# Kernel tuning notes

Measured on AMD Instinct MI355X. Metric: run time of the kernel, lower is better.

The kernel has to match this reference:

```python
import jax, jax.numpy as jnp
import numpy as np
import math

B, TT, TS, C, H, L = 8, 256, 512, 512, 8, 10
HD = C // H
TOPK_FRAME = 64
# layer schedule mirrors MultimodalTransformer.forward tower order:
# 4 stimulus cross-attn (kv=frames, topk), 2 causal self-attn, 2 history cross-attn, 2 causal self-attn
# kv_source: 0=frames, 1=self, 2=id_prev
SCHED = [(0, False, TOPK_FRAME)] * 4 + [(1, True, None)] * 2 + [(2, False, None)] * 2 + [(1, True, None)] * 2


def setup_inputs() -> dict:
    key = jax.random.key(0)
    ks = jax.random.split(key, 4)
    kws = jax.random.split(ks[3], 6)
    w = lambda k, s: jax.random.normal(k, s, jnp.float32) * 0.02
    return {
        "id_x": jax.random.normal(ks[0], (B, TT, C), jnp.float32),
        "id_prev": jax.random.normal(ks[1], (B, TT, C), jnp.float32),
        "frames": jax.random.normal(ks[2], (B, TS, C), jnp.float32),
        "Wq": w(kws[0], (L, C, C)), "bq": jnp.zeros((L, C), jnp.float32),
        "Wk": w(kws[1], (L, C, C)), "bk": jnp.zeros((L, C), jnp.float32),
        "Wv": w(kws[2], (L, C, C)), "bv": jnp.zeros((L, C), jnp.float32),
        "Wo": w(kws[3], (L, C, C)), "bo": jnp.zeros((L, C), jnp.float32),
        "W1": w(kws[4], (L, C, 4 * C)), "b1": jnp.zeros((L, 4 * C), jnp.float32),
        "W2": w(kws[5], (L, 4 * C, C)), "b2": jnp.zeros((L, C), jnp.float32),
        "ln1_g": jnp.ones((L, C), jnp.float32), "ln1_b": jnp.zeros((L, C), jnp.float32),
        "ln2_g": jnp.ones((L, C), jnp.float32), "ln2_b": jnp.zeros((L, C), jnp.float32),
        "lnf_g": jnp.ones((L, C), jnp.float32), "lnf_b": jnp.zeros((L, C), jnp.float32),
    }


def _ln(x, g, b):
    mu = x.mean(-1, keepdims=True)
    var = ((x - mu) ** 2).mean(-1, keepdims=True)
    return (x - mu) * jax.lax.rsqrt(var + 1e-5) * g + b


def _block(x, kv, causal, topk, p):
    # Block.forward: x = x + attn(ln1(x), kv, kv, mask); x = x + mlp(ln2(x)); return ln_f(x)
    Wq, bq, Wk, bk, Wv, bv, Wo, bo, W1, b1, W2, b2, l1g, l1b, l2g, l2b, lfg, lfb = p
    Bx, Tt, Cx = x.shape
    Ts = kv.shape[1]
    h = _ln(x, l1g, l1b)
    q = (h @ Wq + bq).reshape(Bx, Tt, H, HD).transpose(0, 2, 1, 3)   # [B,H,Tt,HD]
    k = (kv @ Wk + bk).reshape(Bx, Ts, H, HD).transpose(0, 2, 1, 3)  # [B,H,Ts,HD]
    v = (kv @ Wv + bv).reshape(Bx, Ts, H, HD).transpose(0, 2, 1, 3)
    att = jnp.einsum('bhqd,bhkd->bhqk', q, k) * (1.0 / math.sqrt(HD))
    if causal:
        m = jnp.tril(jnp.ones((Tt, Ts), dtype=bool))
        att = jnp.where(m, att, -jnp.inf)
    if topk is not None and topk < Ts:
        top = jax.lax.top_k(att, topk)[0]           # [B,H,Tt,topk]
        att = jnp.where(att < top[..., -1:], -jnp.inf, att)
    w_att = jax.nn.softmax(att, axis=-1)
    y = jnp.einsum('bhqk,bhkd->bhqd', w_att, v).transpose(0, 2, 1, 3).reshape(Bx, Tt, Cx)
    x = x + y @ Wo + bo
    h2 = _ln(x, l2g, l2b)
    x = x + jax.nn.gelu(h2 @ W1 + b1, approximate=False) @ W2 + b2
    return _ln(x, lfg, lfb)


def _forward(id_x, id_prev, frames, Wq, bq, Wk, bk, Wv, bv, Wo, bo, W1, b1, W2, b2,
             ln1_g, ln1_b, ln2_g, ln2_b, lnf_g, lnf_b):
    x = id_x
    for i, (src, causal, topk) in enumerate(SCHED):
        kv = (frames, x, id_prev)[src]
        p = (Wq[i], bq[i], Wk[i], bk[i], Wv[i], bv[i], Wo[i], bo[i],
             W1[i], b1[i], W2[i], b2[i],
             ln1_g[i], ln1_b[i], ln2_g[i], ln2_b[i], lnf_g[i], lnf_b[i])
        x = _block(x, kv, causal, topk, p)
    return x


def reference(id_x, id_prev, frames, Wq, bq, Wk, bk, Wv, bv, Wo, bo, W1, b1, W2, b2,
              ln1_g, ln1_b, ln2_g, ln2_b, lnf_g, lnf_b):
    return _forward(id_x, id_prev, frames, Wq, bq, Wk, bk, Wv, bv, Wo, bo, W1, b1, W2, b2,
                    ln1_g, ln1_b, ln2_g, ln2_b, lnf_g, lnf_b)
```

## Files before the change

kernel.cpp:

```cpp
#include <hip/hip_runtime.h>
#include <math.h>

#define CC 512
#define NH 8
#define HD 64
#define TT 256

typedef __attribute__((ext_vector_type(8))) short short8v;
typedef __attribute__((ext_vector_type(4))) float f32x4;

__device__ inline unsigned short bfc(float f) {
  unsigned u = __float_as_uint(f);
  return (unsigned short)((u + 0x7fffu + ((u >> 16) & 1u)) >> 16);
}
__device__ inline float b2f(unsigned short s) {
  return __uint_as_float((unsigned)s << 16);
}
__device__ inline void gld16(const void* g, void* l) {
  __builtin_amdgcn_global_load_lds(
      (const __attribute__((address_space(1))) unsigned int*)g,
      (__attribute__((address_space(3))) unsigned int*)l, 16, 0, 0);
}

__global__ __launch_bounds__(256) void prep_k(const float* __restrict__ id_x,
    const float* __restrict__ frames, const float* __restrict__ id_prev,
    float* __restrict__ x, unsigned short* __restrict__ fb,
    unsigned short* __restrict__ pb) {
  int i = blockIdx.x * 256 + threadIdx.x;
  if (i < 262144) {
    ((float4*)x)[i] = ((const float4*)id_x)[i];
  } else if (i < 786432) {
    int j = i - 262144;
    float4 f = ((const float4*)frames)[j];
    ushort4 o; o.x = bfc(f.x); o.y = bfc(f.y); o.z = bfc(f.z); o.w = bfc(f.w);
    ((ushort4*)fb)[j] = o;
  } else {
    int j = i - 786432;
    float4 f = ((const float4*)id_prev)[j];
    ushort4 o; o.x = bfc(f.x); o.y = bfc(f.y); o.z = bfc(f.z); o.w = bfc(f.w);
    ((ushort4*)pb)[j] = o;
  }
}

__global__ __launch_bounds__(256) void ln_bf(const float* __restrict__ in,
    unsigned short* __restrict__ out, const float* __restrict__ g, const float* __restrict__ b) {
  int row = (blockIdx.x << 2) + (threadIdx.x >> 6), lane = threadIdx.x & 63;
  const float* r = in + (size_t)row * CC;
  float4 v0 = *(const float4*)(r + (lane << 2));
  float4 v1 = *(const float4*)(r + 256 + (lane << 2));
  float s = v0.x + v0.y + v0.z + v0.w + v1.x + v1.y + v1.z + v1.w;
  #pragma unroll
  for (int o = 32; o; o >>= 1) s += __shfl_xor(s, o);
  float mu = s * (1.0f / CC);
  float d0x = v0.x - mu, d0y = v0.y - mu, d0z = v0.z - mu, d0w = v0.w - mu;
  float d1x = v1.x - mu, d1y = v1.y - mu, d1z = v1.z - mu, d1w = v1.w - mu;
  float sq = d0x*d0x + d0y*d0y + d0z*d0z + d0w*d0w + d1x*d1x + d1y*d1y + d1z*d1z + d1w*d1w;
  #pragma unroll
  for (int o = 32; o; o >>= 1) sq += __shfl_xor(sq, o);
  float inv = rsqrtf(sq * (1.0f / CC) + 1e-5f);
  float4 g0 = *(const float4*)(g + (lane << 2)), g1 = *(const float4*)(g + 256 + (lane << 2));
  float4 b0 = *(const float4*)(b + (lane << 2)), b1 = *(const float4*)(b + 256 + (lane << 2));
  ushort4 o0, o1;
  o0.x = bfc(d0x*inv*g0.x + b0.x); o0.y = bfc(d0y*inv*g0.y + b0.y);
  o0.z = bfc(d0z*inv*g0.z + b0.z); o0.w = bfc(d0w*inv*g0.w + b0.w);
  o1.x = bfc(d1x*inv*g1.x + b1.x); o1.y = bfc(d1y*inv*g1.y + b1.y);
  o1.z = bfc(d1z*inv*g1.z + b1.z); o1.w = bfc(d1w*inv*g1.w + b1.w);
  *(ushort4*)(out + (size_t)row * CC + (lane << 2)) = o0;
  *(ushort4*)(out + (size_t)row * CC + 256 + (lane << 2)) = o1;
}

__global__ __launch_bounds__(256) void ln_final(const float* __restrict__ in,
    float* __restrict__ out, const float* __restrict__ g, const float* __restrict__ b) {
  int row = (blockIdx.x << 2) + (threadIdx.x >> 6), lane = threadIdx.x & 63;
  const float* r = in + (size_t)row * CC;
  float4 v0 = *(const float4*)(r + (lane << 2));
  float4 v1 = *(const float4*)(r + 256 + (lane << 2));
  float s = v0.x + v0.y + v0.z + v0.w + v1.x + v1.y + v1.z + v1.w;
  #pragma unroll
  for (int o = 32; o; o >>= 1) s += __shfl_xor(s, o);
  float mu = s * (1.0f / CC);
  float d0x = v0.x - mu, d0y = v0.y - mu, d0z = v0.z - mu, d0w = v0.w - mu;
  float d1x = v1.x - mu, d1y = v1.y - mu, d1z = v1.z - mu, d1w = v1.w - mu;
  float sq = d0x*d0x + d0y*d0y + d0z*d0z + d0w*d0w + d1x*d1x + d1y*d1y + d1z*d1z + d1w*d1w;
  #pragma unroll
  for (int o = 32; o; o >>= 1) sq += __shfl_xor(sq, o);
  float inv = rsqrtf(sq * (1.0f / CC) + 1e-5f);
  float4 g0 = *(const float4*)(g + (lane << 2)), g1 = *(const float4*)(g + 256 + (lane << 2));
  float4 b0 = *(const float4*)(b + (lane << 2)), b1 = *(const float4*)(b + 256 + (lane << 2));
  float4 o0, o1;
  o0.x = d0x*inv*g0.x + b0.x; o0.y = d0y*inv*g0.y + b0.y;
  o0.z = d0z*inv*g0.z + b0.z; o0.w = d0w*inv*g0.w + b0.w;
  o1.x = d1x*inv*g1.x + b1.x; o1.y = d1y*inv*g1.y + b1.y;
  o1.z = d1z*inv*g1.z + b1.z; o1.w = d1w*inv*g1.w + b1.w;
  *(float4*)(out + (size_t)row * CC + (lane << 2)) = o0;
  *(float4*)(out + (size_t)row * CC + 256 + (lane << 2)) = o1;
}

__global__ __launch_bounds__(256) void ln_chain(const float* __restrict__ in,
    float* __restrict__ xout, unsigned short* __restrict__ xb,
    const float* __restrict__ gf, const float* __restrict__ bf,
    const float* __restrict__ g1, const float* __restrict__ b1,
    unsigned short* __restrict__ hout) {
  int row = (blockIdx.x << 2) + (threadIdx.x >> 6), lane = threadIdx.x & 63;
  const float* r = in + (size_t)row * CC;
  float4 v0 = *(const float4*)(r + (lane << 2));
  float4 v1 = *(const float4*)(r + 256 + (lane << 2));
  float s = v0.x + v0.y + v0.z + v0.w + v1.x + v1.y + v1.z + v1.w;
  #pragma unroll
  for (int o = 32; o; o >>= 1) s += __shfl_xor(s, o);
  float mu = s * (1.0f / CC);
  float d0x = v0.x - mu, d0y = v0.y - mu, d0z = v0.z - mu, d0w = v0.w - mu;
  float d1x = v1.x - mu, d1y = v1.y - mu, d1z = v1.z - mu, d1w = v1.w - mu;
  float sq = d0x*d0x + d0y*d0y + d0z*d0z + d0w*d0w + d1x*d1x + d1y*d1y + d1z*d1z + d1w*d1w;
  #pragma unroll
  for (int o = 32; o; o >>= 1) sq += __shfl_xor(sq, o);
  float inv = rsqrtf(sq * (1.0f / CC) + 1e-5f);
  float4 g0 = *(const float4*)(gf + (lane << 2)), g1v = *(const float4*)(gf + 256 + (lane << 2));
  float4 b0 = *(const float4*)(bf + (lane << 2)), b1v = *(const float4*)(bf + 256 + (lane << 2));
  float4 x0, x1;
  x0.x = d0x*inv*g0.x + b0.x; x0.y = d0y*inv*g0.y + b0.y;
  x0.z = d0z*inv*g0.z + b0.z; x0.w = d0w*inv*g0.w + b0.w;
  x1.x = d1x*inv*g1v.x + b1v.x; x1.y = d1y*inv*g1v.y + b1v.y;
  x1.z = d1z*inv*g1v.z + b1v.z; x1.w = d1w*inv*g1v.w + b1v.w;
  *(float4*)(xout + (size_t)row * CC + (lane << 2)) = x0;
  *(float4*)(xout + (size_t)row * CC + 256 + (lane << 2)) = x1;
  ushort4 xb0, xb1;
  xb0.x = bfc(x0.x); xb0.y = bfc(x0.y); xb0.z = bfc(x0.z); xb0.w = bfc(x0.w);
  xb1.x = bfc(x1.x); xb1.y = bfc(x1.y); xb1.z = bfc(x1.z); xb1.w = bfc(x1.w);
  *(ushort4*)(xb + (size_t)row * CC + (lane << 2)) = xb0;
  *(ushort4*)(xb + (size_t)row * CC + 256 + (lane << 2)) = xb1;
  float s2 = x0.x + x0.y + x0.z + x0.w + x1.x + x1.y + x1.z + x1.w;
  #pragma unroll
  for (int o = 32; o; o >>= 1) s2 += __shfl_xor(s2, o);
  float mu2 = s2 * (1.0f / CC);
  float e0x = x0.x - mu2, e0y = x0.y - mu2, e0z = x0.z - mu2, e0w = x0.w - mu2;
  float e1x = x1.x - mu2, e1y = x1.y - mu2, e1z = x1.z - mu2, e1w = x1.w - mu2;
  float sq2 = e0x*e0x + e0y*e0y + e0z*e0z + e0w*e0w + e1x*e1x + e1y*e1y + e1z*e1z + e1w*e1w;
  #pragma unroll
  for (int o = 32; o; o >>= 1) sq2 += __shfl_xor(sq2, o);
  float inv2 = rsqrtf(sq2 * (1.0f / CC) + 1e-5f);
  float4 h0 = *(const float4*)(g1 + (lane << 2)), h1 = *(const float4*)(g1 + 256 + (lane << 2));
  float4 c0 = *(const float4*)(b1 + (lane << 2)), c1 = *(const float4*)(b1 + 256 + (lane << 2));
  ushort4 ho0, ho1;
  ho0.x = bfc(e0x*inv2*h0.x + c0.x); ho0.y = bfc(e0y*inv2*h0.y + c0.y);
  ho0.z = bfc(e0z*inv2*h0.z + c0.z); ho0.w = bfc(e0w*inv2*h0.w + c0.w);
  ho1.x = bfc(e1x*inv2*h1.x + c1.x); ho1.y = bfc(e1y*inv2*h1.y + c1.y);
  ho1.z = bfc(e1z*inv2*h1.z + c1.z); ho1.w = bfc(e1w*inv2*h1.w + c1.w);
  *(ushort4*)(hout + (size_t)row * CC + (lane << 2)) = ho0;
  *(ushort4*)(hout + (size_t)row * CC + 256 + (lane << 2)) = ho1;
}

__global__ __launch_bounds__(256) void transpose_w(
    const float* __restrict__ Wq, const float* __restrict__ Wk,
    const float* __restrict__ Wv, const float* __restrict__ Wo,
    const float* __restrict__ W1, const float* __restrict__ W2,
    int layer_base, unsigned short* __restrict__ wT) {
  int lz = blockIdx.x / 3072;
  int layer = layer_base + lz;
  int bid = blockIdx.x - lz * 3072;
  unsigned short* wTl = wT + (size_t)lz * 3145728;
  const float* src; unsigned short* dst; int R, Cn, tile, lg;
  if (bid < 1024) {
    int seg = bid >> 8; tile = bid & 255; R = 512; Cn = 512; lg = 4;
    const float* s4[4] = {Wq, Wk, Wv, Wo};
    src = s4[seg] + (size_t)layer * 262144;
    dst = wTl + (size_t)seg * 262144;
  } else if (bid < 2048) {
    tile = bid - 1024; R = 512; Cn = 2048; lg = 6;
    src = W1 + (size_t)layer * 1048576; dst = wTl + 1048576;
  } else {
    tile = bid - 2048; R = 2048; Cn = 512; lg = 4;
    src = W2 + (size_t)layer * 1048576; dst = wTl + 2097152;
  }
  int trb = tile >> lg, tcb = tile & ((1 << lg) - 1);
  __shared__ float tl[32][33];
  int t = threadIdx.x;
  int r = t >> 3, c4 = (t & 7) << 2;
  const float* sp = src + (size_t)(trb * 32 + r) * Cn + tcb * 32 + c4;
  float4 fv = *(const float4*)sp;
  tl[r][c4] = fv.x; tl[r][c4 + 1] = fv.y; tl[r][c4 + 2] = fv.z; tl[r][c4 + 3] = fv.w;
  __syncthreads();
  unsigned short* dp = dst + (size_t)(tcb * 32 + r) * R + trb * 32 + c4;
  ushort4 ov;
  ov.x = bfc(tl[c4][r]); ov.y = bfc(tl[c4 + 1][r]);
  ov.z = bfc(tl[c4 + 2][r]); ov.w = bfc(tl[c4 + 3][r]);
  *(ushort4*)dp = ov;
}

template<int BM, int GELU, int RES, int OUTBF, int BIAS2, int QSC>
__global__ __launch_bounds__(256) void gemm_bf(
    const unsigned short* __restrict__ A, const unsigned short* __restrict__ WT,
    const float* __restrict__ bias, const float* __restrict__ bias2,
    void* __restrict__ outp, const float* __restrict__ res, int M, int N, int K) {
  __shared__ __align__(16) unsigned short As[2][BM * 64];
  __shared__ __align__(16) unsigned short Bs[2][64 * 64];
  const int tid = threadIdx.x, lane = tid & 63, wid = tid >> 6;
  const int bm = blockIdx.y * BM, bn = blockIdx.x << 6;
  const int wm = (wid >> 1) * (BM / 2), wn = (wid & 1) << 5;
  constexpr int MF = BM / 32;
  f32x4 acc[MF][2] = {};
  const int fr = lane & 15, fq = lane >> 4;
  const int srow_a = tid >> 3, sgc = tid & 7;

  auto stage = [&](int buf, int k0) {
    #pragma unroll
    for (int i = 0; i < BM / 32; i++) {
      int row = srow_a + (i << 5);
      int gcs = sgc ^ (row & 7);
      gld16(A + (size_t)(bm + row) * K + k0 + (gcs << 3),
            (char*)As[buf] + (i << 12) + (wid << 10));
    }
    #pragma unroll
    for (int i = 0; i < 2; i++) {
      int row = srow_a + (i << 5);
      int gcs = sgc ^ (row & 7);
      gld16(WT + (size_t)(bn + row) * K + k0 + (gcs << 3),
            (char*)Bs[buf] + (i << 12) + (wid << 10));
    }
  };

  stage(0, 0);
  __syncthreads();
  int cur = 0;
  for (int k0 = 0; k0 < K; k0 += 64) {
    if (k0 + 64 < K) stage(cur ^ 1, k0 + 64);
    short8v af[MF][2], bf2[2][2];
    #pragma unroll
    for (int mf = 0; mf < MF; mf++)
      #pragma unroll
      for (int ks = 0; ks < 2; ks++) {
        int r = wm + mf * 16 + fr;
        int c = (ks << 2) + fq;
        af[mf][ks] = *(const short8v*)((const char*)As[cur] + ((((r << 7) + (c << 4))) ^ ((r & 7) << 4)));
      }
    #pragma unroll
    for (int nf = 0; nf < 2; nf++)
      #pragma unroll
      for (int ks = 0; ks < 2; ks++) {
        int r = wn + nf * 16 + fr;
        int c = (ks << 2) + fq;
        bf2[nf][ks] = *(const short8v*)((const char*)Bs[cur] + ((((r << 7) + (c << 4))) ^ ((r & 7) << 4)));
      }
    #pragma unroll
    for (int mf = 0; mf < MF; mf++)
      #pragma unroll
      for (int nf = 0; nf < 2; nf++) {
        acc[mf][nf] = __builtin_amdgcn_mfma_f32_16x16x32_bf16(af[mf][0], bf2[nf][0], acc[mf][nf], 0, 0, 0);
        acc[mf][nf] = __builtin_amdgcn_mfma_f32_16x16x32_bf16(af[mf][1], bf2[nf][1], acc[mf][nf], 0, 0, 0);
      }
    __syncthreads();
    cur ^= 1;
  }
  #pragma unroll
  for (int mf = 0; mf < MF; mf++)
    #pragma unroll
    for (int nf = 0; nf < 2; nf++) {
      int col = bn + wn + nf * 16 + fr;
      float bia = (BIAS2 && col >= 512) ? bias2[col - 512] : bias[col];
      #pragma unroll
      for (int rr = 0; rr < 4; rr++) {
        int row = bm + wm + mf * 16 + fq * 4 + rr;
        float vv = acc[mf][nf][rr] + bia;
        if (GELU) vv = 0.5f * vv * (1.0f + erff(vv * 0.70710678118654752f));
        if (RES)  vv += res[(size_t)row * N + col];
        if (QSC)  vv *= 0.125f;
        if (OUTBF) ((unsigned short*)outp)[(size_t)row * N + col] = bfc(vv);
        else       ((float*)outp)[(size_t)row * N + col] = vv;
      }
    }
}

__global__ __launch_bounds__(256) void gemm_qkv(
    const unsigned short* __restrict__ hb, const unsigned short* __restrict__ wqT,
    const float* __restrict__ bq,
    const unsigned short* __restrict__ kvA, const unsigned short* __restrict__ wkvT,
    const float* __restrict__ bk, const float* __restrict__ bv,
    unsigned short* __restrict__ qout, unsigned short* __restrict__ kvout) {
  const int tid = threadIdx.x, lane = tid & 63, wid = tid >> 6;
  int bid = blockIdx.x;
  const unsigned short *A, *WT;
  const float *bias, *bias2;
  unsigned short* outp;
  int bm, bn, N;
  bool isq = bid < 256;
  if (isq) {
    A = hb; WT = wqT; bias = bq; bias2 = bq; outp = qout; N = 512;
    bm = (bid >> 3) << 6; bn = (bid & 7) << 6;
  } else {
    int t = bid - 256;
    A = kvA; WT = wkvT; bias = bk; bias2 = bv; outp = kvout; N = 1024;
    bm = (t >> 4) << 6; bn = (t & 15) << 6;
  }
  __shared__ __align__(16) unsigned short As[2][64 * 64];
  __shared__ __align__(16) unsigned short Bs[2][64 * 64];
  const int wm = (wid >> 1) << 5, wn = (wid & 1) << 5;
  f32x4 acc[2][2] = {};
  const int fr = lane & 15, fq = lane >> 4;
  const int srow_a = tid >> 3, sgc = tid & 7;
  auto stage = [&](int buf, int k0) {
    #pragma unroll
    for (int i = 0; i < 2; i++) {
      int row = srow_a + (i << 5);
      int gcs = sgc ^ (row & 7);
      gld16(A + (size_t)(bm + row) * 512 + k0 + (gcs << 3),
            (char*)As[buf] + (i << 12) + (wid << 10));
      gld16(WT + (size_t)(bn + row) * 512 + k0 + (gcs << 3),
            (char*)Bs[buf] + (i << 12) + (wid << 10));
    }
  };
  stage(0, 0);
  __syncthreads();
  int cur = 0;
  for (int k0 = 0; k0 < 512; k0 += 64) {
    if (k0 + 64 < 512) stage(cur ^ 1, k0 + 64);
    short8v af[2][2], bf2[2][2];
    #pragma unroll
    for (int mf = 0; mf < 2; mf++)
      #pragma unroll
      for (int ks = 0; ks < 2; ks++) {
        int r = wm + mf * 16 + fr;
        int c = (ks << 2) + fq;
        af[mf][ks] = *(const short8v*)((const char*)As[cur] + ((((r << 7) + (c << 4))) ^ ((r & 7) << 4)));
        int r2 = wn + mf * 16 + fr;
        bf2[mf][ks] = *(const short8v*)((const char*)Bs[cur] + ((((r2 << 7) + (c << 4))) ^ ((r2 & 7) << 4)));
      }
    #pragma unroll
    for (int mf = 0; mf < 2; mf++)
      #pragma unroll
      for (int nf = 0; nf < 2; nf++) {
        acc[mf][nf] = __builtin_amdgcn_mfma_f32_16x16x32_bf16(af[mf][0], bf2[nf][0], acc[mf][nf], 0, 0, 0);
        acc[mf][nf] = __builtin_amdgcn_mfma_f32_16x16x32_bf16(af[mf][1], bf2[nf][1], acc[mf][nf], 0, 0, 0);
      }
    __syncthreads();
    cur ^= 1;
  }
  #pragma unroll
  for (int mf = 0; mf < 2; mf++)
    #pragma unroll
    for (int nf = 0; nf < 2; nf++) {
      int col = bn + wn + nf * 16 + fr;
      float bia = (col >= 512) ? bias2[col - 512] : bias[col];
      #pragma unroll
      for (int rr = 0; rr < 4; rr++) {
        int row = bm + wm + mf * 16 + fq * 4 + rr;
        float vv = acc[mf][nf][rr] + bia;
        if (isq) vv *= 0.125f;
        outp[(size_t)row * N + col] = bfc(vv);
      }
    }
}

template<int CAUSAL, int TOPK, int TSK>
__global__ __launch_bounds__(512, 4) void attn_m(
    const unsigned short* __restrict__ qb, const unsigned short* __restrict__ kv,
    unsigned short* __restrict__ yb) {
  constexpr int NT = TSK / 64;
  constexpr int NKC = TSK / 128;
  constexpr int SST = TSK + 8;
  constexpr int SBYTES = 8 * SST * 4;
  __shared__ __align__(16) char sm[SBYTES + 32768 + 2048];
  float* S = (float*)sm;
  char* KsB = sm + SBYTES;
  char* Qs  = sm + SBYTES + 32768;
  float* swt = (float*)KsB;
  unsigned short* kidx = (unsigned short*)(KsB + 4096);
  int tid = threadIdx.x, lane = tid & 63, wid = tid >> 6;
  int bid = blockIdx.x;
  int swz = ((bid & 7) << 8) | (bid >> 3);
  int b = swz >> 8, h = (swz >> 5) & 7, q0 = (swz & 31) << 3;
  if (tid < 64) {
    int row = tid >> 3, sp = tid & 7;
    gld16(qb + (size_t)((b << 8) + q0 + row) * CC + (h << 6) + ((sp ^ (row & 7)) << 3),
          Qs);
  } else if (tid < 128) {
    short8v z = {0, 0, 0, 0, 0, 0, 0, 0};
    *(short8v*)(Qs + (tid << 4)) = z;
  }
  const unsigned short* kgb = kv + (size_t)b * TSK * 1024 + (h << 6);
  int nte = NKC;
  if (CAUSAL) { int ub = (q0 + 8 + 127) >> 7; nte = ub < NKC ? ub : NKC; }
  auto stageK = [&](int buf, int t) {
    #pragma unroll
    for (int j = 0; j < 2; j++) {
      int s = (wid << 7) + (j << 6) + lane;
      int row = s >> 3, sp = s & 7;
      gld16(kgb + (size_t)((t << 7) + row) * 1024 + ((sp ^ (row & 7)) << 3),
            KsB + (buf << 14) + (wid << 11) + (j << 10));
    }
  };
  stageK(0, 0);
  __syncthreads();
  short8v aF[2];
  {
    int r = lane & 15, kq2 = lane >> 4;
    #pragma unroll
    for (int kc2 = 0; kc2 < 2; kc2++)
      aF[kc2] = *(const short8v*)(Qs +
                 (((r << 7) + (kc2 << 6) + (kq2 << 4)) ^ ((r & 7) << 4)));
  }
  int cur = 0;
  for (int t = 0; t < nte; t++) {
    if (t + 1 < nte) stageK(cur ^ 1, t + 1);
    int kq2 = lane >> 4;
    f32x4 acc = {};
    int key16 = (wid << 4) + (lane & 15);
    #pragma unroll
    for (int kc2 = 0; kc2 < 2; kc2++) {
      short8v bF = *(const short8v*)(KsB + (cur << 14) +
                    (((key16 << 7) + (kc2 << 6) + (kq2 << 4)) ^ ((key16 & 7) << 4)));
      acc = __builtin_amdgcn_mfma_f32_16x16x32_bf16(aF[kc2], bF, acc, 0, 0, 0);
    }
    if (kq2 < 2) {
      int col = (t << 7) + key16;
      #pragma unroll
      for (int r = 0; r < 4; r++)
        S[(kq2 * 4 + r) * SST + col] = acc[r];
    }
    __syncthreads();
    cur ^= 1;
  }
  int row = wid;
  int qi = q0 + row;
  int jmax = CAUSAL ? (qi + 1) : TSK;
  const unsigned short* vgb = kv + (size_t)b * TSK * 1024 + 512 + (h << 6) + lane;
  float sc[NT];
  float lmax = -3.0e38f;
  #pragma unroll
  for (int tt = 0; tt < NT; tt++) {
    int key = lane + (tt << 6);
    float v = (!CAUSAL || key < jmax) ? S[row * SST + key] : -3.0e38f;
    sc[tt] = v;
    lmax = fmaxf(lmax, v);
  }
  float mx = lmax;
  #pragma unroll
  for (int o = 32; o; o >>= 1) mx = fmaxf(mx, __shfl_xor(mx, o));
  float oacc = 0.f;
  if (TOPK) {
    unsigned key[NT];
    #pragma unroll
    for (int tt = 0; tt < NT; tt++) {
      unsigned u = __float_as_uint(sc[tt]);
      key[tt] = (u & 0x80000000u) ? ~u : (u | 0x80000000u);
    }
    unsigned prefix = 0u;
    for (int bit = 31; bit >= 0; bit--) {
      unsigned cand = prefix | (1u << bit);
      int cnt = 0;
      #pragma unroll
      for (int tt = 0; tt < NT; tt++)
        cnt += __popcll(__ballot(key[tt] >= cand));
      if (cnt >= 64) {
        prefix = cand;
        if (cnt == 64) break;
      }
    }
    float wvv[NT];
    float psum = 0.f;
    int basec = 0;
    #pragma unroll
    for (int tt = 0; tt < NT; tt++) {
      bool keep = key[tt] >= prefix;
      float wv = keep ? exp2f((sc[tt] - mx) * 1.4426950408889634f) : 0.f;
      wvv[tt] = wv;
      psum += wv;
      unsigned long long mask = __ballot(keep);
      if (keep) {
        int pos = basec + (int)__popcll(mask & ((1ull << lane) - 1ull));
        if (pos < 128) {
          kidx[(row << 7) + pos] = (unsigned short)(lane + (tt << 6));
          swt[(row << 7) + pos] = wv;
        }
      }
      basec += (int)__popcll(mask);
    }
    #pragma unroll
    for (int o = 32; o; o >>= 1) psum += __shfl_xor(psum, o);
    float inv = 1.0f / psum;
    int nk = basec;
    if (nk <= 128) {
      float a0 = 0.f, a1 = 0.f, a2 = 0.f, a3 = 0.f;
      int i = 0;
      for (; i + 3 < nk; i += 4) {
        a0 += swt[(row << 7) + i]     * b2f(vgb[(size_t)kidx[(row << 7) + i] * 1024]);
        a1 += swt[(row << 7) + i + 1] * b2f(vgb[(size_t)kidx[(row << 7) + i + 1] * 1024]);
        a2 += swt[(row << 7) + i + 2] * b2f(vgb[(size_t)kidx[(row << 7) + i + 2] * 1024]);
        a3 += swt[(row << 7) + i + 3] * b2f(vgb[(size_t)kidx[(row << 7) + i + 3] * 1024]);
      }
      for (; i < nk; i++) a0 += swt[(row << 7) + i] * b2f(vgb[(size_t)kidx[(row << 7) + i] * 1024]);
      oacc = (a0 + a1 + a2 + a3) * inv;
    } else {
      #pragma unroll
      for (int tt = 0; tt < NT; tt++)
        S[row * SST + lane + (tt << 6)] = wvv[tt];
      float a0 = 0.f, a1 = 0.f;
      for (int j = 0; j + 1 < TSK; j += 2) {
        a0 += S[row * SST + j]     * b2f(vgb[(size_t)j * 1024]);
        a1 += S[row * SST + j + 1] * b2f(vgb[(size_t)(j + 1) * 1024]);
      }
      oacc = (a0 + a1) * inv;
    }
  } else {
    float psum = 0.f;
    #pragma unroll
    for (int tt = 0; tt < NT; tt++) {
      int keyj = lane + (tt << 6);
      float wv = (keyj < jmax) ? exp2f((sc[tt] - mx) * 1.4426950408889634f) : 0.f;
      S[row * SST + keyj] = wv;
      psum += wv;
    }
    #pragma unroll
    for (int o = 32; o; o >>= 1) psum += __shfl_xor(psum, o);
    float inv = 1.0f / psum;
    float a0 = 0.f, a1 = 0.f, a2 = 0.f, a3 = 0.f;
    int j = 0;
    for (; j + 3 < jmax; j += 4) {
      a0 += S[row * SST + j]     * b2f(vgb[(size_t)j * 1024]);
      a1 += S[row * SST + j + 1] * b2f(vgb[(size_t)(j + 1) * 1024]);
      a2 += S[row * SST + j + 2] * b2f(vgb[(size_t)(j + 2) * 1024]);
      a3 += S[row * SST + j + 3] * b2f(vgb[(size_t)(j + 3) * 1024]);
    }
    for (; j < jmax; j++) a0 += S[row * SST + j] * b2f(vgb[(size_t)j * 1024]);
    oacc = (a0 + a1 + a2 + a3) * inv;
  }
  yb[(size_t)((b << 8) + qi) * CC + (h << 6) + lane] = bfc(oacc);
}

extern "C" void kernel_launch(void* const* d_in, const int* in_sizes, int n_in,
                              void* d_out, int out_size, void* d_ws, size_t ws_size,
                              hipStream_t stream) {
  const float* id_x    = (const float*)d_in[0];
  const float* id_prev = (const float*)d_in[1];
  const float* frames  = (const float*)d_in[2];
  const float* Wq = (const float*)d_in[3];  const float* bq = (const float*)d_in[4];
  const float* Wk = (const float*)d_in[5];  const float* bk = (const float*)d_in[6];
  const float* Wv = (const float*)d_in[7];  const float* bv = (const float*)d_in[8];
  const float* Wo = (const float*)d_in[9];  const float* bo = (const float*)d_in[10];
  const float* W1 = (const float*)d_in[11]; const float* b1 = (const float*)d_in[12];
  const float* W2 = (const float*)d_in[13]; const float* b2 = (const float*)d_in[14];
  const float* l1g = (const float*)d_in[15]; const float* l1b = (const float*)d_in[16];
  const float* l2g = (const float*)d_in[17]; const float* l2b = (const float*)d_in[18];
  const float* lfg = (const float*)d_in[19]; const float* lfb = (const float*)d_in[20];

  float* x = (float*)d_out;
  char* W  = (char*)d_ws;
  unsigned short* qbuf = (unsigned short*)W;
  unsigned short* kvb  = (unsigned short*)(W + ((size_t)4  << 20));
  unsigned short* m1b  = (unsigned short*)(W + ((size_t)4  << 20));
  unsigned short* hb   = (unsigned short*)(W + ((size_t)12 << 20));
  unsigned short* ybf  = (unsigned short*)(W + ((size_t)14 << 20));
  unsigned short* xb   = (unsigned short*)(W + ((size_t)16 << 20));
  unsigned short* fb   = (unsigned short*)(W + ((size_t)18 << 20));
  unsigned short* pb   = (unsigned short*)(W + ((size_t)22 << 20));
  unsigned short* wT   = (unsigned short*)(W + ((size_t)24 << 20));

  const bool allw = ws_size >= (((size_t)24 << 20) + (size_t)10 * 3145728 * 2);

  prep_k<<<4096, 256, 0, stream>>>(id_x, frames, id_prev, x, fb, pb);
  if (allw)
    transpose_w<<<30720, 256, 0, stream>>>(Wq, Wk, Wv, Wo, W1, W2, 0, wT);

  static const int ssrc[10] = {0, 0, 0, 0, 1, 1, 2, 2, 1, 1};

  for (int i = 0; i < 10; i++) {
    if (!allw)
      transpose_w<<<3072, 256, 0, stream>>>(Wq, Wk, Wv, Wo, W1, W2, i, wT);
    unsigned short* wTl = wT + (allw ? (size_t)i * 3145728 : 0);
    unsigned short* wqT = wTl;
    unsigned short* wkvT = wTl + 262144;
    unsigned short* woT = wTl + 786432;
    unsigned short* w1T = wTl + 1048576;
    unsigned short* w2T = wTl + 2097152;

    if (i == 0)
      ln_bf<<<512, 256, 0, stream>>>(x, hb, l1g, l1b);

    const unsigned short* kvsrc; int Mkv;
    if (ssrc[i] == 0)      { kvsrc = fb; Mkv = 4096; }
    else if (ssrc[i] == 1) { kvsrc = xb; Mkv = 2048; }
    else                   { kvsrc = pb; Mkv = 2048; }
    gemm_qkv<<<256 + (Mkv / 64) * 16, 256, 0, stream>>>(
        hb, wqT, bq + i * 512, kvsrc, wkvT, bk + i * 512, bv + i * 512, qbuf, kvb);

    if (ssrc[i] == 0)      attn_m<0, 1, 512><<<2048, 512, 0, stream>>>(qbuf, kvb, ybf);
    else if (ssrc[i] == 1) attn_m<1, 0, 256><<<2048, 512, 0, stream>>>(qbuf, kvb, ybf);
    else                   attn_m<0, 0, 256><<<2048, 512, 0, stream>>>(qbuf, kvb, ybf);

    gemm_bf<32, 0, 1, 0, 0, 0><<<dim3(8, 64), 256, 0, stream>>>(ybf, woT, bo + i * 512, nullptr, x, x, 2048, 512, 512);
    ln_bf<<<512, 256, 0, stream>>>(x, hb, l2g + i * 512, l2b + i * 512);
    gemm_bf<128, 1, 0, 1, 0, 0><<<dim3(32, 16), 256, 0, stream>>>(hb, w1T, b1 + i * 2048, nullptr, m1b, nullptr, 2048, 2048, 512);
    gemm_bf<32, 0, 1, 0, 0, 0><<<dim3(8, 64), 256, 0, stream>>>(m1b, w2T, b2 + i * 512, nullptr, x, x, 2048, 512, 2048);

    if (i < 9)
      ln_chain<<<512, 256, 0, stream>>>(x, x, xb, lfg + i * 512, lfb + i * 512,
                                        l1g + (i + 1) * 512, l1b + (i + 1) * 512, hb);
    else
      ln_final<<<512, 256, 0, stream>>>(x, x, lfg + i * 512, lfb + i * 512);
  }
}
```

Baseline: 1.016 ms.

## Fuse LayerNorm into the prologue of the Q projection and MLP-up GEMMs

Removes the standalone ln_bf launches and the second LayerNorm from ln_chain. The Q-projection GEMM and a new gemm_ln kernel for the MLP-up projection now compute per-row mean and variance from the fp32 residual and normalize A tiles in registers before writing bf16 into LDS. This saves launches and the round trip through the bf16 hb buffer. In exchange, every N-tile block recomputes row statistics and reads fp32 A instead of bf16 A. The MLP-up GEMM also moves from 128-row to 64-row tiles, and variance is now computed in one pass as E[x^2]-mu^2.

```diff
diff --git a/kernel.cpp b/kernel.cpp
--- a/kernel.cpp
+++ b/kernel.cpp
@@ -40,33 +40,6 @@
     ushort4 o; o.x = bfc(f.x); o.y = bfc(f.y); o.z = bfc(f.z); o.w = bfc(f.w);
     ((ushort4*)pb)[j] = o;
   }
-}
-
-__global__ __launch_bounds__(256) void ln_bf(const float* __restrict__ in,
-    unsigned short* __restrict__ out, const float* __restrict__ g, const float* __restrict__ b) {
-  int row = (blockIdx.x << 2) + (threadIdx.x >> 6), lane = threadIdx.x & 63;
-  const float* r = in + (size_t)row * CC;
-  float4 v0 = *(const float4*)(r + (lane << 2));
-  float4 v1 = *(const float4*)(r + 256 + (lane << 2));
-  float s = v0.x + v0.y + v0.z + v0.w + v1.x + v1.y + v1.z + v1.w;
-  #pragma unroll
-  for (int o = 32; o; o >>= 1) s += __shfl_xor(s, o);
-  float mu = s * (1.0f / CC);
-  float d0x = v0.x - mu, d0y = v0.y - mu, d0z = v0.z - mu, d0w = v0.w - mu;
-  float d1x = v1.x - mu, d1y = v1.y - mu, d1z = v1.z - mu, d1w = v1.w - mu;
-  float sq = d0x*d0x + d0y*d0y + d0z*d0z + d0w*d0w + d1x*d1x + d1y*d1y + d1z*d1z + d1w*d1w;
-  #pragma unroll
-  for (int o = 32; o; o >>= 1) sq += __shfl_xor(sq, o);
-  float inv = rsqrtf(sq * (1.0f / CC) + 1e-5f);
-  float4 g0 = *(const float4*)(g + (lane << 2)), g1 = *(const float4*)(g + 256 + (lane << 2));
-  float4 b0 = *(const float4*)(b + (lane << 2)), b1 = *(const float4*)(b + 256 + (lane << 2));
-  ushort4 o0, o1;
-  o0.x = bfc(d0x*inv*g0.x + b0.x); o0.y = bfc(d0y*inv*g0.y + b0.y);
-  o0.z = bfc(d0z*inv*g0.z + b0.z); o0.w = bfc(d0w*inv*g0.w + b0.w);
-  o1.x = bfc(d1x*inv*g1.x + b1.x); o1.y = bfc(d1y*inv*g1.y + b1.y);
-  o1.z = bfc(d1z*inv*g1.z + b1.z); o1.w = bfc(d1w*inv*g1.w + b1.w);
-  *(ushort4*)(out + (size_t)row * CC + (lane << 2)) = o0;
-  *(ushort4*)(out + (size_t)row * CC + 256 + (lane << 2)) = o1;
 }
 
 __global__ __launch_bounds__(256) void ln_final(const float* __restrict__ in,
@@ -98,9 +71,7 @@
 
 __global__ __launch_bounds__(256) void ln_chain(const float* __restrict__ in,
     float* __restrict__ xout, unsigned short* __restrict__ xb,
-    const float* __restrict__ gf, const float* __restrict__ bf,
-    const float* __restrict__ g1, const float* __restrict__ b1,
-    unsigned short* __restrict__ hout) {
+    const float* __restrict__ gf, const float* __restrict__ bf) {
   int row = (blockIdx.x << 2) + (threadIdx.x >> 6), lane = threadIdx.x & 63;
   const float* r = in + (size_t)row * CC;
   float4 v0 = *(const float4*)(r + (lane << 2));
@@ -129,25 +100,6 @@
   xb1.x = bfc(x1.x); xb1.y = bfc(x1.y); xb1.z = bfc(x1.z); xb1.w = bfc(x1.w);
   *(ushort4*)(xb + (size_t)row * CC + (lane << 2)) = xb0;
   *(ushort4*)(xb + (size_t)row * CC + 256 + (lane << 2)) = xb1;
-  float s2 = x0.x + x0.y + x0.z + x0.w + x1.x + x1.y + x1.z + x1.w;
-  #pragma unroll
-  for (int o = 32; o; o >>= 1) s2 += __shfl_xor(s2, o);
-  float mu2 = s2 * (1.0f / CC);
-  float e0x = x0.x - mu2, e0y = x0.y - mu2, e0z = x0.z - mu2, e0w = x0.w - mu2;
-  float e1x = x1.x - mu2, e1y = x1.y - mu2, e1z = x1.z - mu2, e1w = x1.w - mu2;
-  float sq2 = e0x*e0x + e0y*e0y + e0z*e0z + e0w*e0w + e1x*e1x + e1y*e1y + e1z*e1z + e1w*e1w;
-  #pragma unroll
-  for (int o = 32; o; o >>= 1) sq2 += __shfl_xor(sq2, o);
-  float inv2 = rsqrtf(sq2 * (1.0f / CC) + 1e-5f);
-  float4 h0 = *(const float4*)(g1 + (lane << 2)), h1 = *(const float4*)(g1 + 256 + (lane << 2));
-  float4 c0 = *(const float4*)(b1 + (lane << 2)), c1 = *(const float4*)(b1 + 256 + (lane << 2));
-  ushort4 ho0, ho1;
-  ho0.x = bfc(e0x*inv2*h0.x + c0.x); ho0.y = bfc(e0y*inv2*h0.y + c0.y);
-  ho0.z = bfc(e0z*inv2*h0.z + c0.z); ho0.w = bfc(e0w*inv2*h0.w + c0.w);
-  ho1.x = bfc(e1x*inv2*h1.x + c1.x); ho1.y = bfc(e1y*inv2*h1.y + c1.y);
-  ho1.z = bfc(e1z*inv2*h1.z + c1.z); ho1.w = bfc(e1w*inv2*h1.w + c1.w);
-  *(ushort4*)(hout + (size_t)row * CC + (lane << 2)) = ho0;
-  *(ushort4*)(hout + (size_t)row * CC + 256 + (lane << 2)) = ho1;
 }
 
 __global__ __launch_bounds__(256) void transpose_w(
@@ -187,10 +139,10 @@
   *(ushort4*)dp = ov;
 }
 
-template<int BM, int GELU, int RES, int OUTBF, int BIAS2, int QSC>
+template<int BM, int GELU, int RES, int OUTBF>
 __global__ __launch_bounds__(256) void gemm_bf(
     const unsigned short* __restrict__ A, const unsigned short* __restrict__ WT,
-    const float* __restrict__ bias, const float* __restrict__ bias2,
+    const float* __restrict__ bias,
     void* __restrict__ outp, const float* __restrict__ res, int M, int N, int K) {
   __shared__ __align__(16) unsigned short As[2][BM * 64];
   __shared__ __align__(16) unsigned short Bs[2][64 * 64];
@@ -256,63 +208,95 @@
     #pragma unroll
     for (int nf = 0; nf < 2; nf++) {
       int col = bn + wn + nf * 16 + fr;
-      float bia = (BIAS2 && col >= 512) ? bias2[col - 512] : bias[col];
+      float bia = bias[col];
       #pragma unroll
       for (int rr = 0; rr < 4; rr++) {
         int row = bm + wm + mf * 16 + fq * 4 + rr;
         float vv = acc[mf][nf][rr] + bia;
         if (GELU) vv = 0.5f * vv * (1.0f + erff(vv * 0.70710678118654752f));
         if (RES)  vv += res[(size_t)row * N + col];
-        if (QSC)  vv *= 0.125f;
         if (OUTBF) ((unsigned short*)outp)[(size_t)row * N + col] = bfc(vv);
         else       ((float*)outp)[(size_t)row * N + col] = vv;
       }
     }
 }
 
-__global__ __launch_bounds__(256) void gemm_qkv(
-    const unsigned short* __restrict__ hb, const unsigned short* __restrict__ wqT,
-    const float* __restrict__ bq,
-    const unsigned short* __restrict__ kvA, const unsigned short* __restrict__ wkvT,
-    const float* __restrict__ bk, const float* __restrict__ bv,
-    unsigned short* __restrict__ qout, unsigned short* __restrict__ kvout) {
-  const int tid = threadIdx.x, lane = tid & 63, wid = tid >> 6;
-  int bid = blockIdx.x;
-  const unsigned short *A, *WT;
-  const float *bias, *bias2;
-  unsigned short* outp;
-  int bm, bn, N;
-  bool isq = bid < 256;
-  if (isq) {
-    A = hb; WT = wqT; bias = bq; bias2 = bq; outp = qout; N = 512;
-    bm = (bid >> 3) << 6; bn = (bid & 7) << 6;
-  } else {
-    int t = bid - 256;
-    A = kvA; WT = wkvT; bias = bk; bias2 = bv; outp = kvout; N = 1024;
-    bm = (t >> 4) << 6; bn = (t & 15) << 6;
-  }
+template<int GELU, int OUTBF, int QSC>
+__global__ __launch_bounds__(256) void gemm_ln(
+    const float* __restrict__ xf, const float* __restrict__ lng,
+    const float* __restrict__ lnb, const unsigned short* __restrict__ WT,
+    const float* __restrict__ bias, void* __restrict__ outp, int N) {
   __shared__ __align__(16) unsigned short As[2][64 * 64];
   __shared__ __align__(16) unsigned short Bs[2][64 * 64];
+  __shared__ float gls[512], bls[512], muv[64], invv[64];
+  const int tid = threadIdx.x, lane = tid & 63, wid = tid >> 6;
+  const int bm = blockIdx.y << 6, bn = blockIdx.x << 6;
   const int wm = (wid >> 1) << 5, wn = (wid & 1) << 5;
   f32x4 acc[2][2] = {};
   const int fr = lane & 15, fq = lane >> 4;
-  const int srow_a = tid >> 3, sgc = tid & 7;
-  auto stage = [&](int buf, int k0) {
+  const int srow_b = tid >> 3, sgc = tid & 7;
+  {
+    int sl = lane & 7;
+    #pragma unroll
+    for (int p = 0; p < 2; p++) {
+      int row = (wid << 4) + (p << 3) + (lane >> 3);
+      const float* rp = xf + (size_t)(bm + row) * 512;
+      float s = 0.f, sq = 0.f;
+      #pragma unroll
+      for (int i = 0; i < 16; i++) {
+        float4 v = *(const float4*)(rp + (i << 5) + (sl << 2));
+        s  += v.x + v.y + v.z + v.w;
+        sq += v.x*v.x + v.y*v.y + v.z*v.z + v.w*v.w;
+      }
+      s  += __shfl_xor(s, 1);  s  += __shfl_xor(s, 2);  s  += __shfl_xor(s, 4);
+      sq += __shfl_xor(sq, 1); sq += __shfl_xor(sq, 2); sq += __shfl_xor(sq, 4);
+      if (sl == 0) {
+        float mu = s * (1.f / 512.f);
+        muv[row] = mu;
+        invv[row] = rsqrtf(sq * (1.f / 512.f) - mu * mu + 1e-5f);
+      }
+    }
+    if (tid < 128) ((float4*)gls)[tid] = ((const float4*)lng)[tid];
+    else           ((float4*)bls)[tid - 128] = ((const float4*)lnb)[tid - 128];
+  }
+  __syncthreads();
+  const int arow = tid >> 2, acg = tid & 3;
+  const float muR = muv[arow], ivR = invv[arow];
+  float4 areg[4];
+  auto loadA = [&](int k0) {
+    #pragma unroll
+    for (int j = 0; j < 4; j++)
+      areg[j] = *(const float4*)(xf + (size_t)(bm + arow) * 512 + k0 + (acg << 4) + (j << 2));
+  };
+  auto writeA = [&](int buf, int k0) {
+    #pragma unroll
+    for (int j = 0; j < 4; j++) {
+      int k = (acg << 4) + (j << 2);
+      float4 g4 = *(const float4*)(gls + k0 + k);
+      float4 b4 = *(const float4*)(bls + k0 + k);
+      ushort4 o;
+      o.x = bfc((areg[j].x - muR) * ivR * g4.x + b4.x);
+      o.y = bfc((areg[j].y - muR) * ivR * g4.y + b4.y);
+      o.z = bfc((areg[j].z - muR) * ivR * g4.z + b4.z);
+      o.w = bfc((areg[j].w - muR) * ivR * g4.w + b4.w);
+      *(ushort4*)((char*)As[buf] + (((arow << 7) + (k << 1)) ^ ((arow & 7) << 4))) = o;
+    }
+  };
+  auto stageB = [&](int buf, int k0) {
     #pragma unroll
     for (int i = 0; i < 2; i++) {
-      int row = srow_a + (i << 5);
+      int row = srow_b + (i << 5);
       int gcs = sgc ^ (row & 7);
-      gld16(A + (size_t)(bm + row) * 512 + k0 + (gcs << 3),
-            (char*)As[buf] + (i << 12) + (wid << 10));
       gld16(WT + (size_t)(bn + row) * 512 + k0 + (gcs << 3),
             (char*)Bs[buf] + (i << 12) + (wid << 10));
     }
   };
-  stage(0, 0);
+  loadA(0); stageB(0, 0); writeA(0, 0);
   __syncthreads();
   int cur = 0;
   for (int k0 = 0; k0 < 512; k0 += 64) {
-    if (k0 + 64 < 512) stage(cur ^ 1, k0 + 64);
+    bool more = (k0 + 64 < 512);
+    if (more) { loadA(k0 + 64); stageB(cur ^ 1, k0 + 64); }
     short8v af[2][2], bf2[2][2];
     #pragma unroll
     for (int mf = 0; mf < 2; mf++)
@@ -331,6 +315,7 @@
         acc[mf][nf] = __builtin_amdgcn_mfma_f32_16x16x32_bf16(af[mf][0], bf2[nf][0], acc[mf][nf], 0, 0, 0);
         acc[mf][nf] = __builtin_amdgcn_mfma_f32_16x16x32_bf16(af[mf][1], bf2[nf][1], acc[mf][nf], 0, 0, 0);
       }
+    if (more) writeA(cur ^ 1, k0 + 64);
     __syncthreads();
     cur ^= 1;
   }
@@ -339,15 +324,189 @@
     #pragma unroll
     for (int nf = 0; nf < 2; nf++) {
       int col = bn + wn + nf * 16 + fr;
-      float bia = (col >= 512) ? bias2[col - 512] : bias[col];
+      float bia = bias[col];
       #pragma unroll
       for (int rr = 0; rr < 4; rr++) {
         int row = bm + wm + mf * 16 + fq * 4 + rr;
         float vv = acc[mf][nf][rr] + bia;
-        if (isq) vv *= 0.125f;
-        outp[(size_t)row * N + col] = bfc(vv);
-      }
-    }
+        if (GELU) vv = 0.5f * vv * (1.0f + erff(vv * 0.70710678118654752f));
+        if (QSC)  vv *= 0.125f;
+        if (OUTBF) ((unsigned short*)outp)[(size_t)row * N + col] = bfc(vv);
+        else       ((float*)outp)[(size_t)row * N + col] = vv;
+      }
+    }
+}
+
+__global__ __launch_bounds__(256) void gemm_qkv(
+    const float* __restrict__ xf, const float* __restrict__ l1g,
+    const float* __restrict__ l1b, const unsigned short* __restrict__ wqT,
+    const float* __restrict__ bq,
+    const unsigned short* __restrict__ kvA, const unsigned short* __restrict__ wkvT,
+    const float* __restrict__ bk, const float* __restrict__ bv,
+    unsigned short* __restrict__ qout, unsigned short* __restrict__ kvout) {
+  __shared__ __align__(16) unsigned short As[2][64 * 64];
+  __shared__ __align__(16) unsigned short Bs[2][64 * 64];
+  __shared__ float gls[512], bls[512], muv[64], invv[64];
+  const int tid = threadIdx.x, lane = tid & 63, wid = tid >> 6;
+  const int bid = blockIdx.x;
+  const bool isq = bid < 256;
+  const int wm = (wid >> 1) << 5, wn = (wid & 1) << 5;
+  f32x4 acc[2][2] = {};
+  const int fr = lane & 15, fq = lane >> 4;
+  const int srow = tid >> 3, sgc = tid & 7;
+
+  if (isq) {
+    const int bm = (bid >> 3) << 6, bn = (bid & 7) << 6;
+    {
+      int sl = lane & 7;
+      #pragma unroll
+      for (int p = 0; p < 2; p++) {
+        int row = (wid << 4) + (p << 3) + (lane >> 3);
+        const float* rp = xf + (size_t)(bm + row) * 512;
+        float s = 0.f, sq = 0.f;
+        #pragma unroll
+        for (int i = 0; i < 16; i++) {
+          float4 v = *(const float4*)(rp + (i << 5) + (sl << 2));
+          s  += v.x + v.y + v.z + v.w;
+          sq += v.x*v.x + v.y*v.y + v.z*v.z + v.w*v.w;
+        }
+        s  += __shfl_xor(s, 1);  s  += __shfl_xor(s, 2);  s  += __shfl_xor(s, 4);
+        sq += __shfl_xor(sq, 1); sq += __shfl_xor(sq, 2); sq += __shfl_xor(sq, 4);
+        if (sl == 0) {
+          float mu = s * (1.f / 512.f);
+          muv[row] = mu;
+          invv[row] = rsqrtf(sq * (1.f / 512.f) - mu * mu + 1e-5f);
+        }
+      }
+      if (tid < 128) ((float4*)gls)[tid] = ((const float4*)l1g)[tid];
+      else           ((float4*)bls)[tid - 128] = ((const float4*)l1b)[tid - 128];
+    }
+    __syncthreads();
+    const int arow = tid >> 2, acg = tid & 3;
+    const float muR = muv[arow], ivR = invv[arow];
+    float4 areg[4];
+    auto loadA = [&](int k0) {
+      #pragma unroll
+      for (int j = 0; j < 4; j++)
+        areg[j] = *(const float4*)(xf + (size_t)(bm + arow) * 512 + k0 + (acg << 4) + (j << 2));
+    };
+    auto writeA = [&](int buf, int k0) {
+      #pragma unroll
+      for (int j = 0; j < 4; j++) {
+        int k = (acg << 4) + (j << 2);
+        float4 g4 = *(const float4*)(gls + k0 + k);
+        float4 b4 = *(const float4*)(bls + k0 + k);
+        ushort4 o;
+        o.x = bfc((areg[j].x - muR) * ivR * g4.x + b4.x);
+        o.y = bfc((areg[j].y - muR) * ivR * g4.y + b4.y);
+        o.z = bfc((areg[j].z - muR) * ivR * g4.z + b4.z);
+        o.w = bfc((areg[j].w - muR) * ivR * g4.w + b4.w);
+        *(ushort4*)((char*)As[buf] + (((arow << 7) + (k << 1)) ^ ((arow & 7) << 4))) = o;
+      }
+    };
+    auto stageB = [&](int buf, int k0) {
+      #pragma unroll
+      for (int i = 0; i < 2; i++) {
+        int row = srow + (i << 5);
+        int gcs = sgc ^ (row & 7);
+        gld16(wqT + (size_t)(bn + row) * 512 + k0 + (gcs << 3),
+              (char*)Bs[buf] + (i << 12) + (wid << 10));
+      }
+    };
+    loadA(0); stageB(0, 0); writeA(0, 0);
+    __syncthreads();
+    int cur = 0;
+    for (int k0 = 0; k0 < 512; k0 += 64) {
+      bool more = (k0 + 64 < 512);
+      if (more) { loadA(k0 + 64); stageB(cur ^ 1, k0 + 64); }
+      short8v af[2][2], bf2[2][2];
+      #pragma unroll
+      for (int mf = 0; mf < 2; mf++)
+        #pragma unroll
+        for (int ks = 0; ks < 2; ks++) {
+          int r = wm + mf * 16 + fr;
+          int c = (ks << 2) + fq;
+          af[mf][ks] = *(const short8v*)((const char*)As[cur] + ((((r << 7) + (c << 4))) ^ ((r & 7) << 4)));
+          int r2 = wn + mf * 16 + fr;
+          bf2[mf][ks] = *(const short8v*)((const char*)Bs[cur] + ((((r2 << 7) + (c << 4))) ^ ((r2 & 7) << 4)));
+        }
+      #pragma unroll
+      for (int mf = 0; mf < 2; mf++)
+        #pragma unroll
+        for (int nf = 0; nf < 2; nf++) {
+          acc[mf][nf] = __builtin_amdgcn_mfma_f32_16x16x32_bf16(af[mf][0], bf2[nf][0], acc[mf][nf], 0, 0, 0);
+          acc[mf][nf] = __builtin_amdgcn_mfma_f32_16x16x32_bf16(af[mf][1], bf2[nf][1], acc[mf][nf], 0, 0, 0);
+        }
+      if (more) writeA(cur ^ 1, k0 + 64);
+      __syncthreads();
+      cur ^= 1;
+    }
+    #pragma unroll
+    for (int mf = 0; mf < 2; mf++)
+      #pragma unroll
+      for (int nf = 0; nf < 2; nf++) {
+        int col = bn + wn + nf * 16 + fr;
+        float bia = bq[col];
+        #pragma unroll
+        for (int rr = 0; rr < 4; rr++) {
+          int row = bm + wm + mf * 16 + fq * 4 + rr;
+          float vv = (acc[mf][nf][rr] + bia) * 0.125f;
+          qout[(size_t)row * 512 + col] = bfc(vv);
+        }
+      }
+  } else {
+    const int t = bid - 256;
+    const int bm = (t >> 4) << 6, bn = (t & 15) << 6;
+    auto stage = [&](int buf, int k0) {
+      #pragma unroll
+      for (int i = 0; i < 2; i++) {
+        int row = srow + (i << 5);
+        int gcs = sgc ^ (row & 7);
+        gld16(kvA + (size_t)(bm + row) * 512 + k0 + (gcs << 3),
+              (char*)As[buf] + (i << 12) + (wid << 10));
+        gld16(wkvT + (size_t)(bn + row) * 512 + k0 + (gcs << 3),
+              (char*)Bs[buf] + (i << 12) + (wid << 10));
+      }
+    };
+    stage(0, 0);
+    __syncthreads();
+    int cur = 0;
+    for (int k0 = 0; k0 < 512; k0 += 64) {
+      if (k0 + 64 < 512) stage(cur ^ 1, k0 + 64);
+      short8v af[2][2], bf2[2][2];
+      #pragma unroll
+      for (int mf = 0; mf < 2; mf++)
+        #pragma unroll
+        for (int ks = 0; ks < 2; ks++) {
+          int r = wm + mf * 16 + fr;
+          int c = (ks << 2) + fq;
+          af[mf][ks] = *(const short8v*)((const char*)As[cur] + ((((r << 7) + (c << 4))) ^ ((r & 7) << 4)));
+          int r2 = wn + mf * 16 + fr;
+          bf2[mf][ks] = *(const short8v*)((const char*)Bs[cur] + ((((r2 << 7) + (c << 4))) ^ ((r2 & 7) << 4)));
+        }
+      #pragma unroll
+      for (int mf = 0; mf < 2; mf++)
+        #pragma unroll
+        for (int nf = 0; nf < 2; nf++) {
+          acc[mf][nf] = __builtin_amdgcn_mfma_f32_16x16x32_bf16(af[mf][0], bf2[nf][0], acc[mf][nf], 0, 0, 0);
+          acc[mf][nf] = __builtin_amdgcn_mfma_f32_16x16x32_bf16(af[mf][1], bf2[nf][1], acc[mf][nf], 0, 0, 0);
+        }
+      __syncthreads();
+      cur ^= 1;
+    }
+    #pragma unroll
+    for (int mf = 0; mf < 2; mf++)
+      #pragma unroll
+      for (int nf = 0; nf < 2; nf++) {
+        int col = bn + wn + nf * 16 + fr;
+        float bia = (col >= 512) ? bv[col - 512] : bk[col];
+        #pragma unroll
+        for (int rr = 0; rr < 4; rr++) {
+          int row = bm + wm + mf * 16 + fq * 4 + rr;
+          kvout[(size_t)row * 1024 + col] = bfc(acc[mf][nf][rr] + bia);
+        }
+      }
+  }
 }
 
 template<int CAUSAL, int TOPK, int TSK>
@@ -547,7 +706,6 @@
   unsigned short* qbuf = (unsigned short*)W;
   unsigned short* kvb  = (unsigned short*)(W + ((size_t)4  << 20));
   unsigned short* m1b  = (unsigned short*)(W + ((size_t)4  << 20));
-  unsigned short* hb   = (unsigned short*)(W + ((size_t)12 << 20));
   unsigned short* ybf  = (unsigned short*)(W + ((size_t)14 << 20));
   unsigned short* xb   = (unsigned short*)(W + ((size_t)16 << 20));
   unsigned short* fb   = (unsigned short*)(W + ((size_t)18 << 20));
@@ -572,28 +730,25 @@
     unsigned short* w1T = wTl + 1048576;
     unsigned short* w2T = wTl + 2097152;
 
-    if (i == 0)
-      ln_bf<<<512, 256, 0, stream>>>(x, hb, l1g, l1b);
-
     const unsigned short* kvsrc; int Mkv;
     if (ssrc[i] == 0)      { kvsrc = fb; Mkv = 4096; }
     else if (ssrc[i] == 1) { kvsrc = xb; Mkv = 2048; }
     else                   { kvsrc = pb; Mkv = 2048; }
     gemm_qkv<<<256 + (Mkv / 64) * 16, 256, 0, stream>>>(
-        hb, wqT, bq + i * 512, kvsrc, wkvT, bk + i * 512, bv + i * 512, qbuf, kvb);
+        x, l1g + i * 512, l1b + i * 512, wqT, bq + i * 512,
+        kvsrc, wkvT, bk + i * 512, bv + i * 512, qbuf, kvb);
 
     if (ssrc[i] == 0)      attn_m<0, 1, 512><<<2048, 512, 0, stream>>>(qbuf, kvb, ybf);
     else if (ssrc[i] == 1) attn_m<1, 0, 256><<<2048, 512, 0, stream>>>(qbuf, kvb, ybf);
     else                   attn_m<0, 0, 256><<<2048, 512, 0, stream>>>(qbuf, kvb, ybf);
 
-    gemm_bf<32, 0, 1, 0, 0, 0><<<dim3(8, 64), 256, 0, stream>>>(ybf, woT, bo + i * 512, nullptr, x, x, 2048, 512, 512);
-    ln_bf<<<512, 256, 0, stream>>>(x, hb, l2g + i * 512, l2b + i * 512);
-    gemm_bf<128, 1, 0, 1, 0, 0><<<dim3(32, 16), 256, 0, stream>>>(hb, w1T, b1 + i * 2048, nullptr, m1b, nullptr, 2048, 2048, 512);
-    gemm_bf<32, 0, 1, 0, 0, 0><<<dim3(8, 64), 256, 0, stream>>>(m1b, w2T, b2 + i * 512, nullptr, x, x, 2048, 512, 2048);
+    gemm_bf<32, 0, 1, 0><<<dim3(8, 64), 256, 0, stream>>>(ybf, woT, bo + i * 512, x, x, 2048, 512, 512);
+    gemm_ln<1, 1, 0><<<dim3(32, 32), 256, 0, stream>>>(x, l2g + i * 512, l2b + i * 512,
+                                                       w1T, b1 + i * 2048, m1b, 2048);
+    gemm_bf<32, 0, 1, 0><<<dim3(8, 64), 256, 0, stream>>>(m1b, w2T, b2 + i * 512, x, x, 2048, 512, 2048);
 
     if (i < 9)
-      ln_chain<<<512, 256, 0, stream>>>(x, x, xb, lfg + i * 512, lfb + i * 512,
-                                        l1g + (i + 1) * 512, l1b + (i + 1) * 512, hb);
+      ln_chain<<<512, 256, 0, stream>>>(x, x, xb, lfg + i * 512, lfb + i * 512);
     else
       ln_final<<<512, 256, 0, stream>>>(x, x, lfg + i * 512, lfb + i * 512);
   }
```

Result: slower. 1.144 ms (+12.6%).
